# Kernel optimization log

Hardware: AMD Instinct MI355X
Metric: run time of the kernel (lower is better)

The kernel has to match this reference:

```python
import jax, jax.numpy as jnp
import numpy as np

N = 200000      # total nodes
NG = 100000     # masked (graph) nodes
NU = N - NG     # unconnected nodes
E = 3200000     # edges (index into graph nodes)
C = 1000000     # candidate pairs


def setup_inputs() -> dict:
    key = jax.random.key(0)
    ks = jax.random.split(key, 16)
    s = 0.1  # weight init scale
    x = jax.random.normal(ks[0], (N, 2), jnp.float32)
    mask = jnp.arange(N) < NG
    candidates = jnp.stack([
        jax.random.randint(ks[1], (C,), 0, NG),
        jax.random.randint(ks[2], (C,), 0, NU),
    ], axis=1).astype(jnp.int32)
    edges = jax.random.randint(ks[3], (2, E), 0, NG).astype(jnp.int32)
    return {
        "x": x, "mask": mask, "candidates": candidates, "edges": edges,
        # GraphConv(2,8): lin_rel on aggregated neighbors, lin_root on self, bias in rel
        "w1_rel": jax.random.normal(ks[4], (2, 8), jnp.float32) * s,
        "w1_root": jax.random.normal(ks[5], (2, 8), jnp.float32) * s,
        "b1": jnp.zeros((8,), jnp.float32),
        # GraphConv(8,16)
        "w2_rel": jax.random.normal(ks[6], (8, 16), jnp.float32) * s,
        "w2_root": jax.random.normal(ks[7], (8, 16), jnp.float32) * s,
        "b2": jnp.zeros((16,), jnp.float32),
        # fc_unconnected: Linear(2,16) (source's Linear(8,16) is inconsistent with 2-dim x)
        "wu": jax.random.normal(ks[8], (2, 16), jnp.float32) * s,
        "bu": jnp.zeros((16,), jnp.float32),
        # fc: Linear(32,64) -> ReLU -> Linear(64,1)
        "wa": jax.random.normal(ks[9], (32, 64), jnp.float32) * s,
        "ba": jnp.zeros((64,), jnp.float32),
        "wb": jax.random.normal(ks[10], (64, 1), jnp.float32) * s,
        "bb": jnp.zeros((1,), jnp.float32),
    }


def graph_conv(h, edges, w_rel, w_root, b, n):
    # PyG GraphConv with aggr='add': out_i = W_rel @ sum_{j->i} h_j + W_root @ h_i + b
    src, dst = edges[0], edges[1]
    agg = jax.ops.segment_sum(h[src], dst, num_segments=n)  # [n, d_in]
    return agg @ w_rel + h @ w_root + b


def reference(x, mask, candidates, edges, w1_rel, w1_root, b1,
              w2_rel, w2_root, b2, wu, bu, wa, ba, wb, bb):
    idx_g = jnp.nonzero(mask, size=NG)[0]      # graph node indices
    idx_u = jnp.nonzero(~mask, size=NU)[0]     # unconnected node indices
    x_unconnected = x[idx_u] @ wu + bu                         # [NU, 16]
    h = jax.nn.relu(graph_conv(x[idx_g], edges, w1_rel, w1_root, b1, NG))  # [NG, 8]
    h = jax.nn.relu(graph_conv(h, edges, w2_rel, w2_root, b2, NG))         # [NG, 16]
    ec = jnp.concatenate([h[candidates[:, 0]], x_unconnected[candidates[:, 1]]], axis=-1)  # [C, 32]
    hid = jax.nn.relu(ec @ wa + ba)            # [C, 64]
    return jnp.squeeze(hid @ wb + bb, -1)      # [C]
```

## Files before the change

kernel.cpp:

```cpp
#include <hip/hip_runtime.h>

#define N_TOT  200000
#define NG_    100000
#define NU_    100000
#define E_CNT  3200000
#define C_CNT  1000000

#define NBUCK  196
#define NBLK   256
#define CHUNK  12500

#define CBLK   250
#define CCHUNK 4000
#define CCH_E  3907


__global__ __launch_bounds__(256) void phaseA_f(const int* __restrict__ dst,
                                                const int* __restrict__ cand,
                                                int* __restrict__ cnt_mat,
                                                int* __restrict__ cnt2) {
    __shared__ int hcnt[NBUCK];
    int t = threadIdx.x;
    if (t < NBUCK) hcnt[t] = 0;
    __syncthreads();
    int beg = blockIdx.x * CHUNK, end = beg + CHUNK;
    for (int e = beg + t; e < end; e += 256)
        atomicAdd(&hcnt[dst[e] >> 9], 1);
    __syncthreads();
    if (t < NBUCK) { cnt_mat[blockIdx.x * NBUCK + t] = hcnt[t]; hcnt[t] = 0; }
    __syncthreads();
    int cbeg = blockIdx.x * CCH_E;
    int cend = min(cbeg + CCH_E, C_CNT);
    for (int e = cbeg + t; e < cend; e += 256)
        atomicAdd(&hcnt[cand[2 * e] >> 9], 1);
    __syncthreads();
    if (t < NBUCK) cnt2[blockIdx.x * NBUCK + t] = hcnt[t];
}

__global__ __launch_bounds__(256) void phaseB1_f(const int* __restrict__ cnt_mat,
                                                 const int* __restrict__ cnt2,
                                                 int* __restrict__ off_mat,
                                                 int* __restrict__ off2,
                                                 int* __restrict__ colsum,
                                                 int* __restrict__ csum2) {
    __shared__ int s[256];
    int t = threadIdx.x;
    int k = blockIdx.x % NBUCK;
    bool is_cand = blockIdx.x >= NBUCK;
    const int* cm = is_cand ? cnt2 : cnt_mat;
    int v = cm[t * NBUCK + k];
    s[t] = v;
    __syncthreads();
    for (int off = 1; off < 256; off <<= 1) {
        int u = (t >= off) ? s[t - off] : 0;
        __syncthreads();
        s[t] += u;
        __syncthreads();
    }
    int* om = is_cand ? off2 : off_mat;
    om[t * NBUCK + k] = s[t] - v;
    if (t == 255) (is_cand ? csum2 : colsum)[k] = s[255];
}

__global__ __launch_bounds__(256) void phaseB2_f(const int* __restrict__ colsum,
                                                 const int* __restrict__ csum2,
                                                 int* __restrict__ bbase,
                                                 int* __restrict__ bbase2,
                                                 const float* __restrict__ wu,
                                                 const float* __restrict__ bu,
                                                 const float* __restrict__ wa,
                                                 const float* __restrict__ ba,
                                                 float* __restrict__ wprep) {
    __shared__ int s[256];
    int t = threadIdx.x;
    int v = (t < NBUCK) ? colsum[t] : 0;
    s[t] = v;
    __syncthreads();
    for (int off = 1; off < 256; off <<= 1) {
        int u = (t >= off) ? s[t - off] : 0;
        __syncthreads();
        s[t] += u;
        __syncthreads();
    }
    if (t < NBUCK) bbase[t] = s[t] - v;
    if (t == NBUCK - 1) bbase[NBUCK] = s[t];
    __syncthreads();
    int v2 = (t < NBUCK) ? csum2[t] : 0;
    s[t] = v2;
    __syncthreads();
    for (int off = 1; off < 256; off <<= 1) {
        int u = (t >= off) ? s[t - off] : 0;
        __syncthreads();
        s[t] += u;
        __syncthreads();
    }
    if (t < NBUCK) bbase2[t] = s[t] - v2;
    if (t == NBUCK - 1) bbase2[NBUCK] = s[t];
    if (t < 64) {
        int j = t;
#pragma unroll
        for (int i = 0; i < 16; i++) wprep[j * 16 + i] = wa[i * 64 + j];
        float c0 = 0.f, c1 = 0.f, bc = ba[j];
#pragma unroll
        for (int k2 = 0; k2 < 16; k2++) {
            float w = wa[(16 + k2) * 64 + j];
            c0 += wu[k2] * w;
            c1 += wu[16 + k2] * w;
            bc += bu[k2] * w;
        }
        wprep[1024 + j] = c0;
        wprep[1088 + j] = c1;
        wprep[1152 + j] = bc;
    }
}

__global__ __launch_bounds__(256) void phaseC_f(const int* __restrict__ src,
                                                const int* __restrict__ dst,
                                                const int* __restrict__ off_mat,
                                                const int* __restrict__ bbase,
                                                const int* __restrict__ cand,
                                                const int* __restrict__ off2,
                                                const int* __restrict__ bbase2,
                                                int* __restrict__ pairs,
                                                int2* __restrict__ sc) {
    __shared__ int loc[NBUCK];
    int t = threadIdx.x;
    if (t < NBUCK) loc[t] = bbase[t] + off_mat[blockIdx.x * NBUCK + t];
    __syncthreads();
    int beg = blockIdx.x * CHUNK, end = beg + CHUNK;
    for (int e = beg + t; e < end; e += 256) {
        int d = dst[e], s = src[e];
        int k = d >> 9;
        int pos = atomicAdd(&loc[k], 1);
        pairs[pos] = (s << 9) | (d & 511);
    }
    __syncthreads();
    if (t < NBUCK) loc[t] = bbase2[t] + off2[blockIdx.x * NBUCK + t];
    __syncthreads();
    int cbeg = blockIdx.x * CCH_E;
    int cend = min(cbeg + CCH_E, C_CNT);
    for (int e = cbeg + t; e < cend; e += 256) {
        int g = cand[2 * e], u = cand[2 * e + 1];
        int k = g >> 9;
        int pos = atomicAdd(&loc[k], 1);
        int w0 = g | (u << 17);
        int w1 = (int)(((unsigned)u >> 15) | ((unsigned)e << 2));
        sc[pos] = make_int2(w0, w1);
    }
}


__global__ __launch_bounds__(256) void phaseA(const int* __restrict__ dst,
                                              int* __restrict__ cnt_mat) {
    __shared__ int hcnt[NBUCK];
    int t = threadIdx.x;
    if (t < NBUCK) hcnt[t] = 0;
    __syncthreads();
    int beg = blockIdx.x * CHUNK, end = beg + CHUNK;
    for (int e = beg + t; e < end; e += 256)
        atomicAdd(&hcnt[dst[e] >> 9], 1);
    __syncthreads();
    if (t < NBUCK) cnt_mat[blockIdx.x * NBUCK + t] = hcnt[t];
}

__global__ __launch_bounds__(256) void phaseB1(const int* __restrict__ cnt_mat,
                                               int* __restrict__ off_mat,
                                               int* __restrict__ colsum) {
    __shared__ int s[256];
    int t = threadIdx.x;
    int k = blockIdx.x;
    int v = cnt_mat[t * NBUCK + k];
    s[t] = v;
    __syncthreads();
    for (int off = 1; off < 256; off <<= 1) {
        int u = (t >= off) ? s[t - off] : 0;
        __syncthreads();
        s[t] += u;
        __syncthreads();
    }
    off_mat[t * NBUCK + k] = s[t] - v;
    if (t == 255) colsum[k] = s[255];
}

__global__ __launch_bounds__(256) void phaseB2(const int* __restrict__ colsum,
                                               int* __restrict__ bbase) {
    __shared__ int s[256];
    int t = threadIdx.x;
    int v = (t < NBUCK) ? colsum[t] : 0;
    s[t] = v;
    __syncthreads();
    for (int off = 1; off < 256; off <<= 1) {
        int u = (t >= off) ? s[t - off] : 0;
        __syncthreads();
        s[t] += u;
        __syncthreads();
    }
    if (t < NBUCK) bbase[t] = s[t] - v;
    if (t == NBUCK - 1) bbase[NBUCK] = s[t];
}

__global__ __launch_bounds__(256) void phaseC(const int* __restrict__ src,
                                              const int* __restrict__ dst,
                                              const int* __restrict__ off_mat,
                                              const int* __restrict__ bbase,
                                              int* __restrict__ pairs) {
    __shared__ int loc[NBUCK];
    int t = threadIdx.x;
    if (t < NBUCK) loc[t] = bbase[t] + off_mat[blockIdx.x * NBUCK + t];
    __syncthreads();
    int beg = blockIdx.x * CHUNK, end = beg + CHUNK;
    for (int e = beg + t; e < end; e += 256) {
        int d = dst[e], s = src[e];
        int k = d >> 9;
        int pos = atomicAdd(&loc[k], 1);
        pairs[pos] = (s << 9) | (d & 511);
    }
}

__global__ void prep_kernel(const float* __restrict__ wu,
                            const float* __restrict__ bu,
                            const float* __restrict__ wa,
                            const float* __restrict__ ba,
                            float* __restrict__ wprep) {
    int j = threadIdx.x;
#pragma unroll
    for (int i = 0; i < 16; i++) wprep[j * 16 + i] = wa[i * 64 + j];
    float c0 = 0.f, c1 = 0.f, bc = ba[j];
#pragma unroll
    for (int k = 0; k < 16; k++) {
        float w = wa[(16 + k) * 64 + j];
        c0 += wu[k] * w;
        c1 += wu[16 + k] * w;
        bc += bu[k] * w;
    }
    wprep[1024 + j] = c0;
    wprep[1088 + j] = c1;
    wprep[1152 + j] = bc;
}

__global__ __launch_bounds__(256) void candA(const int* __restrict__ cand,
                                             int* __restrict__ cnt2) {
    __shared__ int hcnt[NBUCK];
    int t = threadIdx.x;
    if (t < NBUCK) hcnt[t] = 0;
    __syncthreads();
    int beg = blockIdx.x * CCHUNK, end = beg + CCHUNK;
    for (int e = beg + t; e < end; e += 256)
        atomicAdd(&hcnt[cand[2 * e] >> 9], 1);
    __syncthreads();
    if (t < NBUCK) cnt2[blockIdx.x * NBUCK + t] = hcnt[t];
}

__global__ __launch_bounds__(256) void candB1(const int* __restrict__ cnt2,
                                              int* __restrict__ off2,
                                              int* __restrict__ csum2) {
    __shared__ int s[256];
    int t = threadIdx.x;
    int k = blockIdx.x;
    int v = (t < CBLK) ? cnt2[t * NBUCK + k] : 0;
    s[t] = v;
    __syncthreads();
    for (int off = 1; off < 256; off <<= 1) {
        int u = (t >= off) ? s[t - off] : 0;
        __syncthreads();
        s[t] += u;
        __syncthreads();
    }
    if (t < CBLK) off2[t * NBUCK + k] = s[t] - v;
    if (t == 255) csum2[k] = s[255];
}

__global__ __launch_bounds__(256) void candB2(const int* __restrict__ csum2,
                                              int* __restrict__ bbase2) {
    __shared__ int s[256];
    int t = threadIdx.x;
    int v = (t < NBUCK) ? csum2[t] : 0;
    s[t] = v;
    __syncthreads();
    for (int off = 1; off < 256; off <<= 1) {
        int u = (t >= off) ? s[t - off] : 0;
        __syncthreads();
        s[t] += u;
        __syncthreads();
    }
    if (t < NBUCK) bbase2[t] = s[t] - v;
    if (t == NBUCK - 1) bbase2[NBUCK] = s[t];
}

__global__ __launch_bounds__(256) void candC(const int* __restrict__ cand,
                                             const int* __restrict__ off2,
                                             const int* __restrict__ bbase2,
                                             int2* __restrict__ sc) {
    __shared__ int loc[NBUCK];
    int t = threadIdx.x;
    if (t < NBUCK) loc[t] = bbase2[t] + off2[blockIdx.x * NBUCK + t];
    __syncthreads();
    int beg = blockIdx.x * CCHUNK, end = beg + CCHUNK;
    for (int e = beg + t; e < end; e += 256) {
        int g = cand[2 * e], u = cand[2 * e + 1];
        int k = g >> 9;
        int pos = atomicAdd(&loc[k], 1);
        int w0 = g | (u << 17);
        int w1 = (int)(((unsigned)u >> 15) | ((unsigned)e << 2));
        sc[pos] = make_int2(w0, w1);
    }
}


__global__ __launch_bounds__(1024) void phaseD(const int* __restrict__ bbase,
                                               const int* __restrict__ pairs,
                                               int* __restrict__ csr_src,
                                               int* __restrict__ node_off) {
    __shared__ int cnt[512], scn[512], base[512];
    int t = threadIdx.x, k = blockIdx.x;
    if (t < 512) cnt[t] = 0;
    __syncthreads();
    int beg = bbase[k], end = bbase[k + 1];
    for (int e = beg + t; e < end; e += 1024)
        atomicAdd(&cnt[pairs[e] & 511], 1);
    __syncthreads();
    if (t < 512) scn[t] = cnt[t];
    __syncthreads();
    for (int off = 1; off < 512; off <<= 1) {
        int v = 0;
        if (t < 512 && t >= off) v = scn[t - off];
        __syncthreads();
        if (t < 512) scn[t] += v;
        __syncthreads();
    }
    if (t < 512) {
        int bse = beg + scn[t] - cnt[t];
        base[t] = bse;
        node_off[(k << 9) + t] = bse;
    }
    __syncthreads();
    for (int e = beg + t; e < end; e += 1024) {
        int p = pairs[e];
        int pos = atomicAdd(&base[p & 511], 1);
        csr_src[pos] = p >> 9;
    }
}

__global__ __launch_bounds__(256) void conv1_csr(const int* __restrict__ node_off,
                                                 const int* __restrict__ csr_src,
                                                 const float* __restrict__ x,
                                                 const float* __restrict__ w_rel,
                                                 const float* __restrict__ w_root,
                                                 const float* __restrict__ b,
                                                 float* __restrict__ h1) {
    int t = threadIdx.x;
    int n = blockIdx.x * 32 + (t >> 3);
    int l = t & 7;
    int beg = node_off[n], end = node_off[n + 1];
    float a0 = 0.f, a1 = 0.f;
    for (int e = beg + l; e < end; e += 8) {
        int s = csr_src[e];
        float2 xv = *(const float2*)(x + 2 * s);
        a0 += xv.x; a1 += xv.y;
    }
#pragma unroll
    for (int d = 1; d < 8; d <<= 1) {
        a0 += __shfl_xor(a0, d, 64);
        a1 += __shfl_xor(a1, d, 64);
    }
    float2 xn = *(const float2*)(x + 2 * n);
    float v = a0 * w_rel[l] + a1 * w_rel[8 + l]
            + xn.x * w_root[l] + xn.y * w_root[8 + l] + b[l];
    h1[8 * n + l] = fmaxf(v, 0.f);
}

__global__ __launch_bounds__(256) void conv2_csr(const int* __restrict__ node_off,
                                                 const int* __restrict__ csr_src,
                                                 const float* __restrict__ h1,
                                                 const float* __restrict__ w_rel,
                                                 const float* __restrict__ w_root,
                                                 const float* __restrict__ b,
                                                 float* __restrict__ h2) {
    int t = threadIdx.x;
    int n = blockIdx.x * 32 + (t >> 3);
    int l = t & 7;
    int beg = node_off[n], end = node_off[n + 1];
    float acc[8] = {0.f, 0.f, 0.f, 0.f, 0.f, 0.f, 0.f, 0.f};
    for (int e = beg + l; e < end; e += 8) {
        int s = csr_src[e];
        const float4* hp = (const float4*)(h1 + 8 * s);
        float4 v0 = hp[0], v1 = hp[1];
        acc[0] += v0.x; acc[1] += v0.y; acc[2] += v0.z; acc[3] += v0.w;
        acc[4] += v1.x; acc[5] += v1.y; acc[6] += v1.z; acc[7] += v1.w;
    }
#pragma unroll
    for (int d = 1; d < 8; d <<= 1)
#pragma unroll
        for (int j = 0; j < 8; j++)
            acc[j] += __shfl_xor(acc[j], d, 64);
    const float4* hp = (const float4*)(h1 + 8 * n);
    float4 t0 = hp[0], t1 = hp[1];
    float hn[8] = {t0.x, t0.y, t0.z, t0.w, t1.x, t1.y, t1.z, t1.w};
#pragma unroll
    for (int cc = 0; cc < 2; cc++) {
        int c = l + 8 * cc;
        float v = b[c];
#pragma unroll
        for (int j = 0; j < 8; j++)
            v += acc[j] * w_rel[j * 16 + c] + hn[j] * w_root[j * 16 + c];
        h2[16 * n + c] = fmaxf(v, 0.f);
    }
}

__global__ __launch_bounds__(256) void precompA(const float* __restrict__ h2,
                                                const float* __restrict__ wa,
                                                const float* __restrict__ wprep,
                                                float* __restrict__ Ag) {
    int g = blockIdx.x * 256 + threadIdx.x;
    if (g >= NG_) return;
    float h[16];
    const float4* hp = (const float4*)(h2 + 16 * g);
#pragma unroll
    for (int q = 0; q < 4; q++) {
        float4 v = hp[q];
        h[4*q] = v.x; h[4*q+1] = v.y; h[4*q+2] = v.z; h[4*q+3] = v.w;
    }
    float4* op = (float4*)(Ag + 64 * g);
#pragma unroll
    for (int q = 0; q < 16; q++) {
        float4 v;
        v.x = wprep[1152 + 4*q + 0];
        v.y = wprep[1152 + 4*q + 1];
        v.z = wprep[1152 + 4*q + 2];
        v.w = wprep[1152 + 4*q + 3];
#pragma unroll
        for (int i = 0; i < 16; i++) {
            float hi = h[i];
            v.x += hi * wa[i*64 + 4*q + 0];
            v.y += hi * wa[i*64 + 4*q + 1];
            v.z += hi * wa[i*64 + 4*q + 2];
            v.w += hi * wa[i*64 + 4*q + 3];
        }
        op[q] = v;
    }
}

__global__ __launch_bounds__(256) void final_mlp7(const int2* __restrict__ sc,
                                                  const float* __restrict__ Ag,
                                                  const float* __restrict__ x,
                                                  const float* __restrict__ wprep,
                                                  const float* __restrict__ wb,
                                                  const float* __restrict__ bb,
                                                  float* __restrict__ out) {
    int nwg = gridDim.x;
    int xcd = blockIdx.x & 7, pos = blockIdx.x >> 3;
    int q = nwg >> 3, r = nwg & 7;
    int wg = (xcd < r ? xcd * (q + 1) : r * (q + 1) + (xcd - r) * q) + pos;

    int t = threadIdx.x;
    int l = t & 7;
    int grp = t >> 3;
    float4 c0lo = *(const float4*)(wprep + 1024 + 4 * l);
    float4 c0hi = *(const float4*)(wprep + 1024 + 32 + 4 * l);
    float4 c1lo = *(const float4*)(wprep + 1088 + 4 * l);
    float4 c1hi = *(const float4*)(wprep + 1088 + 32 + 4 * l);
    float4 wblo = *(const float4*)(wb + 4 * l);
    float4 wbhi = *(const float4*)(wb + 32 + 4 * l);
    float bb0 = bb[0];

    int base = wg * 256;
#pragma unroll 2
    for (int it = 0; it < 8; ++it) {
        int c = base + it * 32 + grp;
        if (c < C_CNT) {
            int2 w = sc[c];
            unsigned w0 = (unsigned)w.x, w1 = (unsigned)w.y;
            int g   = (int)(w0 & 0x1FFFFu);
            int u   = (int)((w0 >> 17) | ((w1 & 3u) << 15));
            int idx = (int)(w1 >> 2);
            float2 xv = *(const float2*)(x + 2 * (NG_ + u));
            const float* rp = Ag + 64 * g;
            float4 alo = *(const float4*)(rp + 4 * l);
            float4 ahi = *(const float4*)(rp + 32 + 4 * l);
            float acc;
            {
                float v0 = alo.x + xv.x * c0lo.x + xv.y * c1lo.x;
                float v1 = alo.y + xv.x * c0lo.y + xv.y * c1lo.y;
                float v2 = alo.z + xv.x * c0lo.z + xv.y * c1lo.z;
                float v3 = alo.w + xv.x * c0lo.w + xv.y * c1lo.w;
                acc  = fmaxf(v0, 0.f) * wblo.x;
                acc += fmaxf(v1, 0.f) * wblo.y;
                acc += fmaxf(v2, 0.f) * wblo.z;
                acc += fmaxf(v3, 0.f) * wblo.w;
            }
            {
                float v0 = ahi.x + xv.x * c0hi.x + xv.y * c1hi.x;
                float v1 = ahi.y + xv.x * c0hi.y + xv.y * c1hi.y;
                float v2 = ahi.z + xv.x * c0hi.z + xv.y * c1hi.z;
                float v3 = ahi.w + xv.x * c0hi.w + xv.y * c1hi.w;
                acc += fmaxf(v0, 0.f) * wbhi.x;
                acc += fmaxf(v1, 0.f) * wbhi.y;
                acc += fmaxf(v2, 0.f) * wbhi.z;
                acc += fmaxf(v3, 0.f) * wbhi.w;
            }
            acc += __shfl_xor(acc, 1);
            acc += __shfl_xor(acc, 2);
            acc += __shfl_xor(acc, 4);
            if (l == 0) out[idx] = acc + bb0;
        }
    }
}


extern "C" void kernel_launch(void* const* d_in, const int* in_sizes, int n_in,
                              void* d_out, int out_size, void* d_ws, size_t ws_size,
                              hipStream_t stream) {
    const float* x      = (const float*)d_in[0];
    const int*   cand   = (const int*)d_in[2];
    const int*   edges  = (const int*)d_in[3];
    const float* w1_rel = (const float*)d_in[4];
    const float* w1_root= (const float*)d_in[5];
    const float* b1     = (const float*)d_in[6];
    const float* w2_rel = (const float*)d_in[7];
    const float* w2_root= (const float*)d_in[8];
    const float* b2     = (const float*)d_in[9];
    const float* wu     = (const float*)d_in[10];
    const float* bu     = (const float*)d_in[11];
    const float* wa     = (const float*)d_in[12];
    const float* ba     = (const float*)d_in[13];
    const float* wb     = (const float*)d_in[14];
    const float* bb     = (const float*)d_in[15];
    float* out = (float*)d_out;

    const int* src = edges;
    const int* dst = edges + E_CNT;

    int* ws_i = (int*)d_ws;
    int*   cnt_mat  = ws_i;
    int*   off_mat  = ws_i + 50176;
    int*   colsum   = ws_i + 100352;
    int*   bbase    = ws_i + 100608;
    int*   node_off = ws_i + 100864;
    float* wprep    = (float*)(ws_i + 201728);
    int*   pairs    = ws_i + 202944;
    int*   csr_src  = ws_i + 3402944;
    float* h1       = (float*)(ws_i + 6602944);
    float* h2       = (float*)(ws_i + 7402944);
    float* Ag       = (float*)(ws_i + 202944);

    bool ext = ws_size >= (size_t)11103808 * sizeof(int);

    dim3 blk256(256);

    if (ext) {
        int*  cnt2   = ws_i + 9002944;
        int*  off2   = ws_i + 9053120;
        int*  csum2  = ws_i + 9103296;
        int*  bbase2 = ws_i + 9103552;
        int2* sc     = (int2*)(ws_i + 9103808);

        phaseA_f <<<NBLK, blk256, 0, stream>>>(dst, cand, cnt_mat, cnt2);
        phaseB1_f<<<2 * NBUCK, blk256, 0, stream>>>(cnt_mat, cnt2, off_mat, off2,
                                                    colsum, csum2);
        phaseB2_f<<<1, blk256, 0, stream>>>(colsum, csum2, bbase, bbase2,
                                            wu, bu, wa, ba, wprep);
        phaseC_f <<<NBLK, blk256, 0, stream>>>(src, dst, off_mat, bbase,
                                               cand, off2, bbase2, pairs, sc);
        phaseD <<<NBUCK, 1024, 0, stream>>>(bbase, pairs, csr_src, node_off);
        conv1_csr<<<3125, blk256, 0, stream>>>(node_off, csr_src, x, w1_rel, w1_root, b1, h1);
        conv2_csr<<<3125, blk256, 0, stream>>>(node_off, csr_src, h1, w2_rel, w2_root, b2, h2);
        precompA<<<(NG_ + 255) / 256, blk256, 0, stream>>>(h2, wa, wprep, Ag);
        final_mlp7<<<(C_CNT + 255) / 256, blk256, 0, stream>>>(sc, Ag, x, wprep, wb, bb, out);
    } else {
        int*  cnt2   = ws_i;
        int*  off2   = ws_i + 50176;
        int*  csum2  = ws_i + 100352;
        int*  bbase2 = ws_i + 100608;
        int2* sc     = (int2*)(ws_i + 6602944);

        prep_kernel<<<1, 64, 0, stream>>>(wu, bu, wa, ba, wprep);
        phaseA <<<NBLK, blk256, 0, stream>>>(dst, cnt_mat);
        phaseB1<<<NBUCK, blk256, 0, stream>>>(cnt_mat, off_mat, colsum);
        phaseB2<<<1, blk256, 0, stream>>>(colsum, bbase);
        phaseC <<<NBLK, blk256, 0, stream>>>(src, dst, off_mat, bbase, pairs);
        phaseD <<<NBUCK, 1024, 0, stream>>>(bbase, pairs, csr_src, node_off);
        conv1_csr<<<3125, blk256, 0, stream>>>(node_off, csr_src, x, w1_rel, w1_root, b1, h1);
        conv2_csr<<<3125, blk256, 0, stream>>>(node_off, csr_src, h1, w2_rel, w2_root, b2, h2);
        precompA<<<(NG_ + 255) / 256, blk256, 0, stream>>>(h2, wa, wprep, Ag);
        candA <<<CBLK, blk256, 0, stream>>>(cand, cnt2);
        candB1<<<NBUCK, blk256, 0, stream>>>(cnt2, off2, csum2);
        candB2<<<1, blk256, 0, stream>>>(csum2, bbase2);
        candC <<<CBLK, blk256, 0, stream>>>(cand, off2, bbase2, sc);
        final_mlp7<<<(C_CNT + 255) / 256, blk256, 0, stream>>>(sc, Ag, x, wprep, wb, bb, out);
    }
}
```

Measured before the change: 267.6 us.

## Build CSR with global per-node atomic histogram and scatter instead of two-level bucket sort

```diff
diff --git a/kernel.cpp b/kernel.cpp
--- a/kernel.cpp
+++ b/kernel.cpp
@@ -15,20 +15,22 @@
 #define CCH_E  3907
 
 
-__global__ __launch_bounds__(256) void phaseA_f(const int* __restrict__ dst,
-                                                const int* __restrict__ cand,
-                                                int* __restrict__ cnt_mat,
-                                                int* __restrict__ cnt2) {
+__global__ __launch_bounds__(256) void zeroN(int* __restrict__ node_cnt) {
+    int i = blockIdx.x * 256 + threadIdx.x;
+    if (i < NG_) node_cnt[i] = 0;
+}
+
+__global__ __launch_bounds__(256) void histE_f(const int* __restrict__ dst,
+                                               const int* __restrict__ cand,
+                                               int* __restrict__ node_cnt,
+                                               int* __restrict__ cnt2) {
     __shared__ int hcnt[NBUCK];
     int t = threadIdx.x;
     if (t < NBUCK) hcnt[t] = 0;
     __syncthreads();
     int beg = blockIdx.x * CHUNK, end = beg + CHUNK;
     for (int e = beg + t; e < end; e += 256)
-        atomicAdd(&hcnt[dst[e] >> 9], 1);
-    __syncthreads();
-    if (t < NBUCK) { cnt_mat[blockIdx.x * NBUCK + t] = hcnt[t]; hcnt[t] = 0; }
-    __syncthreads();
+        atomicAdd(&node_cnt[dst[e]], 1);
     int cbeg = blockIdx.x * CCH_E;
     int cend = min(cbeg + CCH_E, C_CNT);
     for (int e = cbeg + t; e < cend; e += 256)
@@ -37,18 +39,56 @@
     if (t < NBUCK) cnt2[blockIdx.x * NBUCK + t] = hcnt[t];
 }
 
-__global__ __launch_bounds__(256) void phaseB1_f(const int* __restrict__ cnt_mat,
-                                                 const int* __restrict__ cnt2,
-                                                 int* __restrict__ off_mat,
-                                                 int* __restrict__ off2,
-                                                 int* __restrict__ colsum,
-                                                 int* __restrict__ csum2) {
+__global__ __launch_bounds__(512) void scanMix(const int* __restrict__ node_cnt,
+                                               const int* __restrict__ cnt2,
+                                               int* __restrict__ node_off,
+                                               int* __restrict__ off2,
+                                               int* __restrict__ colsumN,
+                                               int* __restrict__ csum2) {
+    __shared__ int s[512];
+    int t = threadIdx.x;
+    if (blockIdx.x < NBUCK) {
+        int k = blockIdx.x;
+        int idx = (k << 9) + t;
+        int v = (idx < NG_) ? node_cnt[idx] : 0;
+        s[t] = v;
+        __syncthreads();
+        for (int off = 1; off < 512; off <<= 1) {
+            int u = (t >= off) ? s[t - off] : 0;
+            __syncthreads();
+            s[t] += u;
+            __syncthreads();
+        }
+        if (idx < NG_) node_off[idx] = s[t] - v;
+        if (t == 511) colsumN[k] = s[511];
+    } else {
+        int k = blockIdx.x - NBUCK;
+        int v = (t < NBLK) ? cnt2[t * NBUCK + k] : 0;
+        s[t] = v;
+        __syncthreads();
+        for (int off = 1; off < 512; off <<= 1) {
+            int u = (t >= off) ? s[t - off] : 0;
+            __syncthreads();
+            s[t] += u;
+            __syncthreads();
+        }
+        if (t < NBLK) off2[t * NBUCK + k] = s[t] - v;
+        if (t == 511) csum2[k] = s[511];
+    }
+}
+
+__global__ __launch_bounds__(256) void scan2f(const int* __restrict__ colsumN,
+                                              const int* __restrict__ csum2,
+                                              int* __restrict__ bbaseN,
+                                              int* __restrict__ bbase2,
+                                              const float* __restrict__ wu,
+                                              const float* __restrict__ bu,
+                                              const float* __restrict__ wa,
+                                              const float* __restrict__ ba,
+                                              float* __restrict__ wprep) {
     __shared__ int s[256];
     int t = threadIdx.x;
-    int k = blockIdx.x % NBUCK;
-    bool is_cand = blockIdx.x >= NBUCK;
-    const int* cm = is_cand ? cnt2 : cnt_mat;
-    int v = cm[t * NBUCK + k];
+    int v = (t < NBUCK) ? colsumN[t] : 0;
     s[t] = v;
     __syncthreads();
     for (int off = 1; off < 256; off <<= 1) {
@@ -57,33 +97,8 @@
         s[t] += u;
         __syncthreads();
     }
-    int* om = is_cand ? off2 : off_mat;
-    om[t * NBUCK + k] = s[t] - v;
-    if (t == 255) (is_cand ? csum2 : colsum)[k] = s[255];
-}
-
-__global__ __launch_bounds__(256) void phaseB2_f(const int* __restrict__ colsum,
-                                                 const int* __restrict__ csum2,
-                                                 int* __restrict__ bbase,
-                                                 int* __restrict__ bbase2,
-                                                 const float* __restrict__ wu,
-                                                 const float* __restrict__ bu,
-                                                 const float* __restrict__ wa,
-                                                 const float* __restrict__ ba,
-                                                 float* __restrict__ wprep) {
-    __shared__ int s[256];
-    int t = threadIdx.x;
-    int v = (t < NBUCK) ? colsum[t] : 0;
-    s[t] = v;
-    __syncthreads();
-    for (int off = 1; off < 256; off <<= 1) {
-        int u = (t >= off) ? s[t - off] : 0;
-        __syncthreads();
-        s[t] += u;
-        __syncthreads();
-    }
-    if (t < NBUCK) bbase[t] = s[t] - v;
-    if (t == NBUCK - 1) bbase[NBUCK] = s[t];
+    if (t < NBUCK) bbaseN[t] = s[t] - v;
+    if (t == NBUCK - 1) bbaseN[NBUCK] = s[t];
     __syncthreads();
     int v2 = (t < NBUCK) ? csum2[t] : 0;
     s[t] = v2;
@@ -114,27 +129,35 @@
     }
 }
 
-__global__ __launch_bounds__(256) void phaseC_f(const int* __restrict__ src,
+__global__ __launch_bounds__(512) void scan3(int* __restrict__ node_off,
+                                             int* __restrict__ node_fill,
+                                             const int* __restrict__ bbaseN) {
+    int k = blockIdx.x, t = threadIdx.x;
+    int idx = (k << 9) + t;
+    if (idx < NG_) {
+        int v = node_off[idx] + bbaseN[k];
+        node_off[idx] = v;
+        node_fill[idx] = v;
+    }
+    if (k == 0 && t == 0) node_off[NG_] = E_CNT;
+}
+
+__global__ __launch_bounds__(256) void scatterE(const int* __restrict__ src,
                                                 const int* __restrict__ dst,
-                                                const int* __restrict__ off_mat,
-                                                const int* __restrict__ bbase,
-                                                const int* __restrict__ cand,
-                                                const int* __restrict__ off2,
-                                                const int* __restrict__ bbase2,
-                                                int* __restrict__ pairs,
-                                                int2* __restrict__ sc) {
+                                                int* __restrict__ node_fill,
+                                                int* __restrict__ csr_src) {
+    int e = blockIdx.x * 256 + threadIdx.x;
+    int d = dst[e], s = src[e];
+    int pos = atomicAdd(&node_fill[d], 1);
+    csr_src[pos] = s;
+}
+
+__global__ __launch_bounds__(256) void candC_e(const int* __restrict__ cand,
+                                               const int* __restrict__ off2,
+                                               const int* __restrict__ bbase2,
+                                               int2* __restrict__ sc) {
     __shared__ int loc[NBUCK];
     int t = threadIdx.x;
-    if (t < NBUCK) loc[t] = bbase[t] + off_mat[blockIdx.x * NBUCK + t];
-    __syncthreads();
-    int beg = blockIdx.x * CHUNK, end = beg + CHUNK;
-    for (int e = beg + t; e < end; e += 256) {
-        int d = dst[e], s = src[e];
-        int k = d >> 9;
-        int pos = atomicAdd(&loc[k], 1);
-        pairs[pos] = (s << 9) | (d & 511);
-    }
-    __syncthreads();
     if (t < NBUCK) loc[t] = bbase2[t] + off2[blockIdx.x * NBUCK + t];
     __syncthreads();
     int cbeg = blockIdx.x * CCH_E;
@@ -306,7 +329,6 @@
     }
 }
 
-
 __global__ __launch_bounds__(1024) void phaseD(const int* __restrict__ bbase,
                                                const int* __restrict__ pairs,
                                                int* __restrict__ csr_src,
@@ -340,6 +362,7 @@
         csr_src[pos] = p >> 9;
     }
 }
+
 
 __global__ __launch_bounds__(256) void conv1_csr(const int* __restrict__ node_off,
                                                  const int* __restrict__ csr_src,
@@ -543,25 +566,30 @@
     float* h2       = (float*)(ws_i + 7402944);
     float* Ag       = (float*)(ws_i + 202944);
 
-    bool ext = ws_size >= (size_t)11103808 * sizeof(int);
+    bool ext = ws_size >= (size_t)11254144 * sizeof(int);
 
     dim3 blk256(256);
 
     if (ext) {
-        int*  cnt2   = ws_i + 9002944;
-        int*  off2   = ws_i + 9053120;
-        int*  csum2  = ws_i + 9103296;
-        int*  bbase2 = ws_i + 9103552;
-        int2* sc     = (int2*)(ws_i + 9103808);
-
-        phaseA_f <<<NBLK, blk256, 0, stream>>>(dst, cand, cnt_mat, cnt2);
-        phaseB1_f<<<2 * NBUCK, blk256, 0, stream>>>(cnt_mat, cnt2, off_mat, off2,
-                                                    colsum, csum2);
-        phaseB2_f<<<1, blk256, 0, stream>>>(colsum, csum2, bbase, bbase2,
-                                            wu, bu, wa, ba, wprep);
-        phaseC_f <<<NBLK, blk256, 0, stream>>>(src, dst, off_mat, bbase,
-                                               cand, off2, bbase2, pairs, sc);
-        phaseD <<<NBUCK, 1024, 0, stream>>>(bbase, pairs, csr_src, node_off);
+        int*  node_cnt  = ws_i + 9002944;
+        int*  node_fill = ws_i + 9102944;
+        int*  colsumN   = ws_i + 9202944;
+        int*  bbaseN    = ws_i + 9203200;
+        int*  cnt2      = ws_i + 9203456;
+        int*  csum2     = ws_i + 9253632;
+        int*  bbase2    = ws_i + 9253888;
+        int2* sc        = (int2*)(ws_i + 9254144);
+        int*  off2      = off_mat;
+
+        zeroN   <<<(NG_ + 255) / 256, blk256, 0, stream>>>(node_cnt);
+        histE_f <<<NBLK, blk256, 0, stream>>>(dst, cand, node_cnt, cnt2);
+        scanMix <<<2 * NBUCK, dim3(512), 0, stream>>>(node_cnt, cnt2, node_off, off2,
+                                                      colsumN, csum2);
+        scan2f  <<<1, blk256, 0, stream>>>(colsumN, csum2, bbaseN, bbase2,
+                                           wu, bu, wa, ba, wprep);
+        scan3   <<<NBUCK, dim3(512), 0, stream>>>(node_off, node_fill, bbaseN);
+        candC_e <<<NBLK, blk256, 0, stream>>>(cand, off2, bbase2, sc);
+        scatterE<<<E_CNT / 256, blk256, 0, stream>>>(src, dst, node_fill, csr_src);
         conv1_csr<<<3125, blk256, 0, stream>>>(node_off, csr_src, x, w1_rel, w1_root, b1, h1);
         conv2_csr<<<3125, blk256, 0, stream>>>(node_off, csr_src, h1, w2_rel, w2_root, b2, h2);
         precompA<<<(NG_ + 255) / 256, blk256, 0, stream>>>(h2, wa, wprep, Ag);
```

Measured after the change: 613.7 us. +129.3%, slower.
